# Optimization experiments

Measured on AMD Instinct MI355X. Metric: run time of the kernel, lower is better.

The kernel has to match this reference:

```python
import jax, jax.numpy as jnp
import numpy as np

B, T, N, D = 4, 24, 2048, 128
H = 4
HD = D // H
E = 8
K = 2
INTER = 512            # dim * mlp_ratio
MINTER = INTER // K    # per-expert intermediate (512//2 = 256)
EPS = 1e-6
ALPHA = 0.05           # GCN residual mixing
SCALE = HD ** -0.5


def setup_inputs() -> dict:
    key = jax.random.key(0)
    ks = jax.random.split(key, 32)
    w = lambda i, shape: (jax.random.normal(ks[i], shape, jnp.float32) * 0.02)
    inp = {
        "x": jax.random.normal(ks[0], (B, T, N, D), jnp.float32),
        "k": jax.random.normal(ks[1], (B, T, N, D), jnp.float32),
        "v": jax.random.normal(ks[2], (B, T, N, D), jnp.float32),
        "adj": jax.random.uniform(ks[3], (N, N), jnp.float32),
        # attention qkv projections (torch Linear: y = x @ W.T + b)
        "Wq": w(4, (D, D)), "bq": jnp.zeros((D,), jnp.float32),
        "Wk": w(5, (D, D)), "bk": jnp.zeros((D,), jnp.float32),
        "Wv": w(6, (D, D)), "bv": jnp.zeros((D,), jnp.float32),
        "norm_tatt_w": jnp.ones((D,), jnp.float32),
        # GCN
        "gcn_fc1_w": w(7, (D, D)),
        "gcn_mlp_w": w(8, (D, D)), "gcn_mlp_b": jnp.zeros((D,), jnp.float32),
        # block norms
        "norm1_w": jnp.ones((D,), jnp.float32),
        "norm2_w": jnp.ones((D,), jnp.float32),
        # MoE
        "gate_w": w(9, (E, D)),
        "ew1": w(10, (E, MINTER, D)),
        "ew2": w(11, (E, D, MINTER)),
        "ew3": w(12, (E, MINTER, D)),
        "sw1": w(13, (INTER, D)),
        "sw2": w(14, (D, INTER)),
        "sw3": w(15, (INTER, D)),
        "sgate_w": w(16, (1, D)),
    }
    return inp


def rms_norm(x, w):
    var = jnp.mean(x * x, axis=-1, keepdims=True)
    return w * (x * jax.lax.rsqrt(var + EPS))


def swiglu(x, w1, w2, w3):
    return (jax.nn.silu(x @ w1.T) * (x @ w3.T)) @ w2.T


def reference(x, k, v, adj, Wq, bq, Wk, bk, Wv, bv, norm_tatt_w,
              gcn_fc1_w, gcn_mlp_w, gcn_mlp_b, norm1_w, norm2_w,
              gate_w, ew1, ew2, ew3, sw1, sw2, sw3, sgate_w):
    # ---- pre-norm ----
    x_n = rms_norm(x, norm1_w)
    k_n = rms_norm(k, norm1_w)

    # ---- temporal self-attention (per node, over T) ----
    def heads(y, W, b):  # [B,T,N,D] -> [B,N,H,T,hd]
        y = y @ W.T + b
        return y.transpose(0, 2, 1, 3).reshape(B, N, -1, H, HD).transpose(0, 1, 3, 2, 4)

    q = heads(x_n, Wq, bq)
    kk = heads(k_n, Wk, bk)
    vv = heads(k_n, Wv, bv)  # module passes k for both k and v
    attn = jnp.einsum('bnhqd,bnhkd->bnhqk', q, kk) * SCALE
    attn = jax.nn.softmax(attn, axis=-1)
    t_x = jnp.einsum('bnhqk,bnhkd->bnhqd', attn, vv)
    t_x = t_x.transpose(0, 3, 1, 2, 4).reshape(B, T, N, D)  # [B,T,N,D]
    t_x = rms_norm(t_x, norm_tatt_w)

    # ---- GCN: row-normalized adjacency over node axis ----
    a = adj / jnp.sum(adj, axis=1, keepdims=True)            # a[n,k] = adj[n,k]/d[n]
    mixed = jnp.einsum('nk,btkd->btnd', a, t_x)
    gcn_out = mixed @ gcn_fc1_w.T
    out = ALPHA * t_x + (1.0 - ALPHA) * gcn_out
    ho = out @ gcn_mlp_w.T + gcn_mlp_b

    x = x + ho  # residual (drop_path = identity)

    # ---- MoE sparse experts ----
    x2 = rms_norm(x, norm2_w).reshape(-1, D)                 # [Tok, D]
    router_logits = x2 @ gate_w.T                            # [Tok, E]
    rw = jax.nn.softmax(router_logits.astype(jnp.float32), axis=-1)
    top_w, top_idx = jax.lax.top_k(rw, K)                    # [Tok, K]
    top_w = top_w.astype(x2.dtype)

    final = jnp.zeros_like(x2)
    for e in range(E):  # fixed small expert count
        coef = jnp.sum(jnp.where(top_idx == e, top_w, 0.0), axis=-1)  # [Tok]
        final = final + coef[:, None] * swiglu(x2, ew1[e], ew2[e], ew3[e])

    shared = swiglu(x2, sw1, sw2, sw3)
    shared = jax.nn.sigmoid(x2 @ sgate_w.T) * shared
    final = final + shared

    x = x + final.reshape(B, T, N, D)
    return x, router_logits
```

## Files before the change

### kernel.cpp

```cpp
#include <hip/hip_runtime.h>

#define BB 4
#define TT 24
#define NN 2048
#define DD 128
#define HH 4
#define HD 32
#define TOK 196608
#define EE 8
#define MINTER 256
#define INTER 512

typedef unsigned short u16;
typedef __attribute__((ext_vector_type(8))) short  bf16x8;
typedef __attribute__((ext_vector_type(4))) float  f32x4;
typedef __attribute__((ext_vector_type(4))) unsigned int u32x4;

#define MFMA(a,b,c) __builtin_amdgcn_mfma_f32_16x16x32_bf16((a),(b),(c),0,0,0)
#define AS(n) __attribute__((address_space(n)))

static __device__ __forceinline__ u16 f2b(float f) {
    union { float f; unsigned u; } v; v.f = f;
    unsigned r = v.u + 0x7FFFu + ((v.u >> 16) & 1u);
    return (u16)(r >> 16);
}
static __device__ __forceinline__ u16 f2b_fast(float f) {
    union { float f; unsigned u; } v; v.f = f;
    return (u16)(v.u >> 16);
}
static __device__ __forceinline__ float b2f(u16 b) {
    union { unsigned u; float f; } v; v.u = ((unsigned)b) << 16;
    return v.f;
}
static __device__ __forceinline__ float silu_mul(float u, float v) {
    return u * __builtin_amdgcn_rcpf(1.f + __expf(-u)) * v;
}

template<int C>
static __device__ __forceinline__ bf16x8 frag_ld(const u16* s, int row, int kbyte) {
    constexpr int mask = ((C/8) < 8 ? (C/8) : 8) - 1;
    int byte = row * (C * 2) + (kbyte ^ ((row & mask) << 4));
    return *(const bf16x8*)((const char*)s + byte);
}
template<int C>
static __device__ __forceinline__ u16 lds_us(const u16* s, int r, int c) {
    constexpr int mask = ((C/8) < 8 ? (C/8) : 8) - 1;
    int byte = r * (C * 2) + ((((c >> 3) << 4) ^ ((r & mask) << 4))) + ((c & 7) << 1);
    return *(const u16*)((const char*)s + byte);
}
template<int C>
static __device__ __forceinline__ void lds_store_us(u16* s, int r, int c, u16 v) {
    constexpr int mask = ((C/8) < 8 ? (C/8) : 8) - 1;
    int byte = r * (C * 2) + ((((c >> 3) << 4) ^ ((r & mask) << 4))) + ((c & 7) << 1);
    *(u16*)((char*)s + byte) = v;
}
static __device__ __forceinline__ bf16x8 frag_ld_p80(const u16* s, int row, int kbyte) {
    return *(const bf16x8*)((const char*)s + row * 80 + kbyte);
}
static __device__ __forceinline__ void sh_store_p80(u16* s, int r, int c, u16 v) {
    *(u16*)((char*)s + r * 80 + c * 2) = v;
}
template<int C>
static __device__ __forceinline__ void stage_bf16(u16* s, const u16* g, int gstride,
                                                  int rows, int tid, int nthr) {
    constexpr int cpr = C / 8;
    constexpr int mask = (cpr < 8 ? cpr : 8) - 1;
    for (int i = tid; i < rows * cpr; i += nthr) {
        int r = i / cpr, cc = i - r * cpr;
        u32x4 v = *(const u32x4*)(g + (size_t)r * gstride + cc * 8);
        *(u32x4*)((char*)s + r * (C * 2) + ((cc * 16) ^ ((r & mask) << 4))) = v;
    }
}
static __device__ __forceinline__ void stage_rms(u16* sA, const float* __restrict__ in,
        const float* __restrict__ nw, int tid) {
    int wid = tid >> 6, lane = tid & 63;
    float2 wv = *(const float2*)(nw + lane * 2);
    for (int rr = 0; rr < 32; ++rr) {
        int r = wid * 32 + rr;
        float2 v = *(const float2*)(in + (size_t)r * 128 + lane * 2);
        float ss = v.x * v.x + v.y * v.y;
        #pragma unroll
        for (int o = 32; o > 0; o >>= 1) ss += __shfl_xor(ss, o);
        float sc = rsqrtf(ss * (1.f / 128.f) + 1e-6f);
        unsigned pack = ((unsigned)f2b(v.y * sc * wv.y) << 16) | (unsigned)f2b(v.x * sc * wv.x);
        int byte = r * 256 + (((lane >> 2) * 16) ^ ((r & 7) << 4)) + ((lane & 3) << 2);
        *(unsigned*)((char*)sA + byte) = pack;
    }
}
static __device__ __forceinline__ void stage_async64(u16* s, const u16* g, int wi, int lane) {
    int slot = wi * 64 + lane;
    int r = slot >> 3, c = slot & 7;
    const u16* src = g + r * 2048 + ((c ^ (r & 7)) << 3);
    __builtin_amdgcn_global_load_lds((const AS(1) void*)src,
                                     (AS(3) void*)(s + wi * 512), 16, 0, 0);
}
static __device__ __forceinline__ void stage_img16(u16* buf, const u16* img, int wid, int lane) {
    #pragma unroll
    for (int t = 0; t < 4; ++t) {
        int wi = wid + t * 4;
        __builtin_amdgcn_global_load_lds((const AS(1) void*)(img + wi * 512 + lane * 8),
                                         (AS(3) void*)(buf + wi * 512), 16, 0, 0);
    }
}
static __device__ __forceinline__ void zero_acc(f32x4 acc[4][4]) {
    f32x4 z = {0.f, 0.f, 0.f, 0.f};
    #pragma unroll
    for (int i = 0; i < 4; ++i)
        #pragma unroll
        for (int j = 0; j < 4; ++j) acc[i][j] = z;
}
template<int CA, int CB>
static __device__ __forceinline__ void gemm_step64(const u16* sA, const u16* sB,
        int arow0, int brow0, int kbyte, f32x4 acc[4][4], int ln15) {
    bf16x8 a[4], b[4];
    #pragma unroll
    for (int i = 0; i < 4; ++i) a[i] = frag_ld<CA>(sA, arow0 + i * 16 + ln15, kbyte);
    #pragma unroll
    for (int j = 0; j < 4; ++j) b[j] = frag_ld<CB>(sB, brow0 + j * 16 + ln15, kbyte);
    #pragma unroll
    for (int i = 0; i < 4; ++i)
        #pragma unroll
        for (int j = 0; j < 4; ++j)
            acc[i][j] = MFMA(a[i], b[j], acc[i][j]);
}

static __device__ __forceinline__ void swiglu_chunk(const u16* buf, u16* sH,
        const bf16x8 av[2][4], const bf16x8 w2r[8], f32x4 aout[2][8],
        int wid, int g16, int ln15) {
    const u16* W1c = buf;
    const u16* W3c = buf + 4096;
    f32x4 z = {0.f, 0.f, 0.f, 0.f};
    f32x4 a1[2][2], a3[2][2];
    #pragma unroll
    for (int mf = 0; mf < 2; ++mf)
        #pragma unroll
        for (int nf = 0; nf < 2; ++nf) { a1[mf][nf] = z; a3[mf][nf] = z; }
    __builtin_amdgcn_s_setprio(1);
    #pragma unroll
    for (int ks = 0; ks < 4; ++ks) {
        int kb = ks * 64 + g16 * 16;
        #pragma unroll
        for (int nf = 0; nf < 2; ++nf) {
            bf16x8 b1 = frag_ld<128>(W1c, nf * 16 + ln15, kb);
            bf16x8 b3 = frag_ld<128>(W3c, nf * 16 + ln15, kb);
            a1[0][nf] = MFMA(av[0][ks], b1, a1[0][nf]);
            a1[1][nf] = MFMA(av[1][ks], b1, a1[1][nf]);
            a3[0][nf] = MFMA(av[0][ks], b3, a3[0][nf]);
            a3[1][nf] = MFMA(av[1][ks], b3, a3[1][nf]);
        }
    }
    __builtin_amdgcn_s_setprio(0);
    #pragma unroll
    for (int mf = 0; mf < 2; ++mf)
        #pragma unroll
        for (int nf = 0; nf < 2; ++nf)
            #pragma unroll
            for (int r = 0; r < 4; ++r) {
                int row = wid * 32 + mf * 16 + g16 * 4 + r;
                int col = nf * 16 + ln15;
                sh_store_p80(sH, row, col, f2b_fast(silu_mul(a1[mf][nf][r], a3[mf][nf][r])));
            }
    asm volatile("s_waitcnt lgkmcnt(0)" ::: "memory");
    __builtin_amdgcn_sched_barrier(0);
    {
        int kb = g16 * 16;
        bf16x8 ah0 = frag_ld_p80(sH, wid * 32 + ln15, kb);
        bf16x8 ah1 = frag_ld_p80(sH, wid * 32 + 16 + ln15, kb);
        __builtin_amdgcn_s_setprio(1);
        #pragma unroll
        for (int nf = 0; nf < 8; ++nf) {
            aout[0][nf] = MFMA(ah0, w2r[nf], aout[0][nf]);
            aout[1][nf] = MFMA(ah1, w2r[nf], aout[1][nf]);
        }
        __builtin_amdgcn_s_setprio(0);
    }
}

__global__ __launch_bounds__(256) void preconvert(
        const float* __restrict__ Wq, const float* __restrict__ Wk,
        const float* __restrict__ Wv, const float* __restrict__ g1,
        const float* __restrict__ g2,
        const float* __restrict__ e1, const float* __restrict__ e2,
        const float* __restrict__ e3,
        const float* __restrict__ s1, const float* __restrict__ s2,
        const float* __restrict__ s3,
        u16* __restrict__ arena, int* __restrict__ cnts) {
    int idx = blockIdx.x * 256 + threadIdx.x;
    if (blockIdx.x == 0 && threadIdx.x < 8) cnts[threadIdx.x] = 0;
    if (idx < 20480) {
        int s = idx >> 12, rel = idx & 4095;
        const float* src = (s == 0) ? Wq : (s == 1) ? Wk : (s == 2) ? Wv : (s == 3) ? g1 : g2;
        const float4 v = *(const float4*)(src + (size_t)rel * 4);
        union { unsigned long long q; u16 us[4]; } o;
        o.us[0] = f2b(v.x); o.us[1] = f2b(v.y); o.us[2] = f2b(v.z); o.us[3] = f2b(v.w);
        *(unsigned long long*)(arena + (size_t)idx * 4) = o.q;
        return;
    }
    int p = idx - 20480;
    if (p >= 122880) return;
    int imgIdx = p / 1536;
    int ppos = p - imgIdx * 1536;
    const float *w1s, *w3s, *w2s_; int w2stride, ic;
    u16* img;
    if (imgIdx < 64) {
        int e = imgIdx >> 3; ic = imgIdx & 7;
        w1s = e1 + (size_t)e * 32768;
        w3s = e3 + (size_t)e * 32768;
        w2s_ = e2 + (size_t)e * 32768;
        w2stride = 256;
        img = arena + 81920 + (size_t)imgIdx * 12288;
    } else {
        ic = imgIdx - 64;
        w1s = s1; w3s = s3; w2s_ = s2; w2stride = 512;
        img = arena + 868352 + (size_t)ic * 12288;
    }
    const float* src;
    if (ppos < 1024) {
        const float* wsrc = (ppos < 512) ? w1s : w3s;
        int pp = ppos & 511;
        int r = pp >> 4, chq = pp & 15;
        int cc = chq ^ (r & 7);
        src = wsrc + (size_t)(ic * 32 + r) * 128 + cc * 8;
    } else {
        int q = ppos - 1024;
        int nf = q >> 6, ln = q & 63;
        int l15 = ln & 15, g = ln >> 4;
        src = w2s_ + (size_t)(nf * 16 + l15) * w2stride + ic * 32 + g * 8;
    }
    union { u32x4 v; u16 us[8]; } o;
    #pragma unroll
    for (int j = 0; j < 8; ++j) o.us[j] = f2b(src[j]);
    *(u32x4*)(img + (size_t)ppos * 8) = o.v;
}

__global__ __launch_bounds__(256) void proj_rms(
        const float* __restrict__ xin, const u16* __restrict__ W,
        const float* __restrict__ bias, const float* __restrict__ nw,
        u16* __restrict__ out) {
    int tok0 = blockIdx.x * 128;
    __shared__ u16 sA[128 * 128];
    __shared__ u16 sW[128 * 128];
    int tid = threadIdx.x, lane = tid & 63, ln15 = lane & 15, g16 = lane >> 4, wid = tid >> 6;
    int wm = (wid >> 1) * 64, wn = (wid & 1) * 64;
    stage_rms(sA, xin + (size_t)tok0 * 128, nw, tid);
    stage_bf16<128>(sW, W, 128, 128, tid, 256);
    __syncthreads();
    f32x4 acc[4][4];
    zero_acc(acc);
    #pragma unroll
    for (int ks = 0; ks < 4; ++ks)
        gemm_step64<128, 128>(sA, sW, wm, wn, ks * 64 + g16 * 16, acc, ln15);
    #pragma unroll
    for (int j = 0; j < 4; ++j) {
        int col = wn + j * 16 + ln15;
        float bv = bias[col];
        #pragma unroll
        for (int i = 0; i < 4; ++i)
            #pragma unroll
            for (int r = 0; r < 4; ++r) {
                int row = wm + i * 16 + g16 * 4 + r;
                out[(size_t)(tok0 + row) * 128 + col] = f2b(acc[i][j][r] + bv);
            }
    }
}

__global__ __launch_bounds__(256) void projkv_rms(
        const float* __restrict__ kin, const u16* __restrict__ Wk,
        const float* __restrict__ bk, const u16* __restrict__ Wv,
        const float* __restrict__ bv, const float* __restrict__ nw,
        u16* __restrict__ kout, u16* __restrict__ vout) {
    int tok0 = blockIdx.x * 128;
    __shared__ u16 sA[128 * 128];
    __shared__ u16 sW[128 * 128];
    int tid = threadIdx.x, lane = tid & 63, ln15 = lane & 15, g16 = lane >> 4, wid = tid >> 6;
    int wm = (wid >> 1) * 64, wn = (wid & 1) * 64;
    stage_rms(sA, kin + (size_t)tok0 * 128, nw, tid);
    stage_bf16<128>(sW, Wk, 128, 128, tid, 256);
    __syncthreads();
    f32x4 acc[4][4];
    zero_acc(acc);
    #pragma unroll
    for (int ks = 0; ks < 4; ++ks)
        gemm_step64<128, 128>(sA, sW, wm, wn, ks * 64 + g16 * 16, acc, ln15);
    #pragma unroll
    for (int j = 0; j < 4; ++j) {
        int col = wn + j * 16 + ln15;
        float bvv = bk[col];
        #pragma unroll
        for (int i = 0; i < 4; ++i)
            #pragma unroll
            for (int r = 0; r < 4; ++r) {
                int row = wm + i * 16 + g16 * 4 + r;
                kout[(size_t)(tok0 + row) * 128 + col] = f2b(acc[i][j][r] + bvv);
            }
    }
    __syncthreads();
    stage_bf16<128>(sW, Wv, 128, 128, tid, 256);
    __syncthreads();
    zero_acc(acc);
    #pragma unroll
    for (int ks = 0; ks < 4; ++ks)
        gemm_step64<128, 128>(sA, sW, wm, wn, ks * 64 + g16 * 16, acc, ln15);
    #pragma unroll
    for (int j = 0; j < 4; ++j) {
        int col = wn + j * 16 + ln15;
        float bvv = bv[col];
        #pragma unroll
        for (int i = 0; i < 4; ++i)
            #pragma unroll
            for (int r = 0; r < 4; ++r) {
                int row = wm + i * 16 + g16 * 4 + r;
                vout[(size_t)(tok0 + row) * 128 + col] = f2b(acc[i][j][r] + bvv);
            }
    }
}

__global__ __launch_bounds__(256) void attn_kernel(
        const u16* __restrict__ q, const u16* __restrict__ kk, const u16* __restrict__ vv,
        const float* __restrict__ ntw, u16* __restrict__ txn) {
    int bid = blockIdx.x;
    int b = bid >> 11;
    int n = bid & 2047;
    __shared__ u16 sQ[4][24][32];
    __shared__ u16 sK[4][24][32];
    __shared__ u16 sV[4][24][32];
    __shared__ float sS[4][24][24];
    __shared__ float sO[24][128];
    int tid = threadIdx.x, lane = tid & 63, wid = tid >> 6;
    for (int idx = tid; idx < 3072; idx += 256) {
        int h = idx / 768;
        int rem = idx - h * 768;
        int t = rem >> 5;
        int d = rem & 31;
        size_t off = ((size_t)((b * 24 + t) * 2048 + n)) * 128 + h * 32 + d;
        sQ[h][t][d] = q[off];
        sK[h][t][d] = kk[off];
        sV[h][t][d] = vv[off];
    }
    __syncthreads();
    int h = wid;
    for (int i = lane; i < 576; i += 64) {
        int qi = i / 24, ki = i - qi * 24;
        float s = 0.f;
        #pragma unroll
        for (int c = 0; c < 32; ++c) s += b2f(sQ[h][qi][c]) * b2f(sK[h][ki][c]);
        sS[h][qi][ki] = s * 0.17677669529663687f;
    }
    __syncthreads();
    if (lane < 24) {
        float m = -1e30f;
        #pragma unroll
        for (int c = 0; c < 24; ++c) m = fmaxf(m, sS[h][lane][c]);
        float e[24]; float sum = 0.f;
        #pragma unroll
        for (int c = 0; c < 24; ++c) { e[c] = __expf(sS[h][lane][c] - m); sum += e[c]; }
        float inv = 1.f / sum;
        #pragma unroll
        for (int c = 0; c < 24; ++c) sS[h][lane][c] = e[c] * inv;
    }
    __syncthreads();
    for (int i = lane; i < 768; i += 64) {
        int qi = i >> 5, d = i & 31;
        float acc = 0.f;
        #pragma unroll
        for (int c = 0; c < 24; ++c) acc += sS[h][qi][c] * b2f(sV[h][c][d]);
        sO[qi][h * 32 + d] = acc;
    }
    __syncthreads();
    for (int j = 0; j < 6; ++j) {
        int t = wid * 6 + j;
        float v0 = sO[t][lane], v1 = sO[t][lane + 64];
        float ss = v0 * v0 + v1 * v1;
        #pragma unroll
        for (int o = 32; o > 0; o >>= 1) ss += __shfl_xor(ss, o);
        float sc = rsqrtf(ss * (1.f / 128.f) + 1e-6f);
        size_t off = ((size_t)((b * 24 + t) * 2048 + n)) * 128;
        txn[off + lane]      = f2b(v0 * sc * ntw[lane]);
        txn[off + lane + 64] = f2b(v1 * sc * ntw[lane + 64]);
    }
}

__global__ __launch_bounds__(256) void adj_norm(const float* __restrict__ adj, u16* __restrict__ abf) {
    int nrow = blockIdx.x;
    const float* r = adj + (size_t)nrow * 2048;
    int tid = threadIdx.x;
    float s = 0.f;
    for (int c = tid; c < 2048; c += 256) s += r[c];
    __shared__ float red[4];
    #pragma unroll
    for (int o = 32; o > 0; o >>= 1) s += __shfl_xor(s, o);
    if ((tid & 63) == 0) red[tid >> 6] = s;
    __syncthreads();
    float inv = 1.f / (red[0] + red[1] + red[2] + red[3]);
    u16* o = abf + (size_t)nrow * 2048;
    for (int c = tid; c < 2048; c += 256) o[c] = f2b(r[c] * inv);
}

__global__ __launch_bounds__(256) void transpose_k(const u16* __restrict__ txn, u16* __restrict__ txT) {
    int bt = blockIdx.x >> 5;
    int n0 = (blockIdx.x & 31) * 64;
    int tid = threadIdx.x;
    int nn = tid & 63, dg = tid >> 6;
    for (int rep = 0; rep < 4; ++rep) {
        int d0 = rep * 32 + dg * 8;
        union { u32x4 v; u16 us[8]; } u;
        u.v = *(const u32x4*)(txn + ((size_t)(bt * 2048 + n0 + nn)) * 128 + d0);
        #pragma unroll
        for (int j = 0; j < 8; ++j)
            txT[((size_t)(bt * 128 + d0 + j)) * 2048 + n0 + nn] = u.us[j];
    }
}

__global__ __launch_bounds__(256) void gcn_gemm(
        const u16* __restrict__ abf, const u16* __restrict__ txT, u16* __restrict__ mixed) {
    int bt = blockIdx.x >> 4;
    int n0 = (blockIdx.x & 15) * 128;
    __shared__ u16 sA[128 * 64];
    __shared__ u16 sB[128 * 64];
    int tid = threadIdx.x, lane = tid & 63, ln15 = lane & 15, g16 = lane >> 4, wid = tid >> 6;
    int wm = (wid >> 1) * 64, wn = (wid & 1) * 64;
    f32x4 acc[4][4];
    zero_acc(acc);
    const u16* aRow = abf + (size_t)n0 * 2048;
    const u16* bRow = txT + (size_t)bt * 128 * 2048;
    for (int k0 = 0; k0 < 2048; k0 += 64) {
        __syncthreads();
        #pragma unroll
        for (int i = 0; i < 4; ++i) stage_async64(sA, aRow + k0, wid * 4 + i, lane);
        #pragma unroll
        for (int i = 0; i < 4; ++i) stage_async64(sB, bRow + k0, wid * 4 + i, lane);
        __syncthreads();
        #pragma unroll
        for (int ks = 0; ks < 2; ++ks)
            gemm_step64<64, 64>(sA, sB, wm, wn, ks * 64 + g16 * 16, acc, ln15);
    }
    u16* out = mixed + ((size_t)(bt * 2048 + n0)) * 128;
    #pragma unroll
    for (int i = 0; i < 4; ++i)
        #pragma unroll
        for (int j = 0; j < 4; ++j)
            #pragma unroll
            for (int r = 0; r < 4; ++r) {
                int row = wm + i * 16 + g16 * 4 + r;
                int col = wn + j * 16 + ln15;
                out[(size_t)row * 128 + col] = f2b(acc[i][j][r]);
            }
}

__global__ __launch_bounds__(256) void fused_gcn_router(
        const u16* __restrict__ mixed, const u16* __restrict__ txn,
        const float* __restrict__ x,
        const u16* __restrict__ W1, const u16* __restrict__ W2,
        const float* __restrict__ bias2, const float* __restrict__ n2w,
        const float* __restrict__ gatew,
        float* __restrict__ outx, float* __restrict__ outlog,
        u16* __restrict__ x2n,
        int* __restrict__ lists, float* __restrict__ listw, int* __restrict__ cnts) {
    int tok0 = blockIdx.x * 128;
    __shared__ char LB[65536];
    __shared__ float sGate[1024];
    __shared__ float sN2[128];
    __shared__ float sBias[128];
    __shared__ float sLog[1024];
    __shared__ float sPart[256];
    __shared__ float sScale[128];
    __shared__ int sBCnt[8];
    __shared__ int sGBase[8];
    u16* sM = (u16*)LB;
    u16* sW = (u16*)(LB + 32768);
    float* sXn = (float*)LB;
    int tid = threadIdx.x, lane = tid & 63, ln15 = lane & 15, g16 = lane >> 4, wid = tid >> 6;
    int wm = (wid >> 1) * 64, wn = (wid & 1) * 64;
    stage_bf16<128>(sM, mixed + (size_t)tok0 * 128, 128, 128, tid, 256);
    stage_bf16<128>(sW, W1, 128, 128, tid, 256);
    for (int i = tid; i < 1024; i += 256) sGate[i] = gatew[i];
    if (tid < 128) { sN2[tid] = n2w[tid]; sBias[tid] = bias2[tid]; }
    if (tid < 8) sBCnt[tid] = 0;
    __syncthreads();
    f32x4 acc[4][4];
    zero_acc(acc);
    #pragma unroll
    for (int ks = 0; ks < 4; ++ks)
        gemm_step64<128, 128>(sM, sW, wm, wn, ks * 64 + g16 * 16, acc, ln15);
    __syncthreads();
    stage_bf16<128>(sM, txn + (size_t)tok0 * 128, 128, 128, tid, 256);
    stage_bf16<128>(sW, W2, 128, 128, tid, 256);
    __syncthreads();
    #pragma unroll
    for (int i = 0; i < 4; ++i)
        #pragma unroll
        for (int j = 0; j < 4; ++j)
            #pragma unroll
            for (int r = 0; r < 4; ++r) {
                int row = wm + i * 16 + g16 * 4 + r;
                int col = wn + j * 16 + ln15;
                float tv = b2f(lds_us<128>(sM, row, col));
                lds_store_us<128>(sM, row, col, f2b(0.05f * tv + 0.95f * acc[i][j][r]));
            }
    __syncthreads();
    zero_acc(acc);
    #pragma unroll
    for (int ks = 0; ks < 4; ++ks)
        gemm_step64<128, 128>(sM, sW, wm, wn, ks * 64 + g16 * 16, acc, ln15);
    #pragma unroll
    for (int i = 0; i < 4; ++i)
        #pragma unroll
        for (int j = 0; j < 4; ++j)
            #pragma unroll
            for (int r = 0; r < 4; ++r) {
                int row = wm + i * 16 + g16 * 4 + r;
                int col = wn + j * 16 + ln15;
                float xv = x[(size_t)(tok0 + row) * 128 + col] + acc[i][j][r] + sBias[col];
                outx[(size_t)(tok0 + row) * 128 + col] = xv;
                acc[i][j][r] = xv;
            }
    #pragma unroll
    for (int i = 0; i < 4; ++i)
        #pragma unroll
        for (int r = 0; r < 4; ++r) {
            float s = 0.f;
            #pragma unroll
            for (int j = 0; j < 4; ++j) s += acc[i][j][r] * acc[i][j][r];
            s += __shfl_xor(s, 1); s += __shfl_xor(s, 2);
            s += __shfl_xor(s, 4); s += __shfl_xor(s, 8);
            if (ln15 == 0) sPart[(wm + i * 16 + g16 * 4 + r) * 2 + (wid & 1)] = s;
        }
    __syncthreads();
    if (tid < 128)
        sScale[tid] = rsqrtf((sPart[tid * 2] + sPart[tid * 2 + 1]) * (1.f / 128.f) + 1e-6f);
    __syncthreads();
    #pragma unroll
    for (int i = 0; i < 4; ++i)
        #pragma unroll
        for (int j = 0; j < 4; ++j)
            #pragma unroll
            for (int r = 0; r < 4; ++r) {
                int row = wm + i * 16 + g16 * 4 + r;
                int col = wn + j * 16 + ln15;
                sXn[row * 128 + col] = acc[i][j][r] * sScale[row] * sN2[col];
            }
    __syncthreads();
    {
        int r = tid >> 1, e0 = (tid & 1) * 4;
        float a0 = 0, a1 = 0, a2 = 0, a3 = 0;
        for (int cc = 0; cc < 128; ++cc) {
            int c = (cc + r) & 127;
            float v = sXn[r * 128 + c];
            a0 += v * sGate[(e0 + 0) * 128 + c];
            a1 += v * sGate[(e0 + 1) * 128 + c];
            a2 += v * sGate[(e0 + 2) * 128 + c];
            a3 += v * sGate[(e0 + 3) * 128 + c];
        }
        int rb = r * 8 + e0;
        sLog[rb + 0] = a0; sLog[rb + 1] = a1; sLog[rb + 2] = a2; sLog[rb + 3] = a3;
        size_t ob = (size_t)(tok0 + r) * 8 + e0;
        outlog[ob + 0] = a0; outlog[ob + 1] = a1; outlog[ob + 2] = a2; outlog[ob + 3] = a3;
    }
    for (int cc = tid; cc < 2048; cc += 256) {
        int r = cc >> 4, c0 = (cc & 15) * 8;
        union { u32x4 v; u16 us[8]; } u;
        #pragma unroll
        for (int jj = 0; jj < 8; ++jj) u.us[jj] = f2b(sXn[r * 128 + c0 + jj]);
        *(u32x4*)(x2n + (size_t)(tok0 + r) * 128 + c0) = u.v;
    }
    __syncthreads();
    int e1 = 0, e2 = 0, le1 = 0, le2 = 0;
    float w1v = 0.f, w2v = 0.f;
    if (tid < 128) {
        int r = tid;
        float l[8];
        #pragma unroll
        for (int e = 0; e < 8; ++e) l[e] = sLog[r * 8 + e];
        float m = l[0];
        #pragma unroll
        for (int e = 1; e < 8; ++e) m = fmaxf(m, l[e]);
        float ex[8]; float s = 0.f;
        #pragma unroll
        for (int e = 0; e < 8; ++e) { ex[e] = __expf(l[e] - m); s += ex[e]; }
        float inv = 1.f / s;
        float b1v = ex[0]; e1 = 0;
        #pragma unroll
        for (int e = 1; e < 8; ++e) if (ex[e] > b1v) { b1v = ex[e]; e1 = e; }
        e2 = (e1 == 0) ? 1 : 0; float b2v = ex[e2];
        #pragma unroll
        for (int e = 0; e < 8; ++e) if (e != e1 && ex[e] > b2v) { b2v = ex[e]; e2 = e; }
        w1v = b1v * inv; w2v = b2v * inv;
        le1 = atomicAdd(&sBCnt[e1], 1);
        le2 = atomicAdd(&sBCnt[e2], 1);
    }
    __syncthreads();
    if (tid < 8) sGBase[tid] = atomicAdd(&cnts[tid], sBCnt[tid]);
    __syncthreads();
    if (tid < 128) {
        int tok = tok0 + tid;
        int p1 = sGBase[e1] + le1;
        lists[(size_t)e1 * TOK + p1] = tok * 2 + 0; listw[(size_t)e1 * TOK + p1] = w1v;
        int p2 = sGBase[e2] + le2;
        lists[(size_t)e2 * TOK + p2] = tok * 2 + 1; listw[(size_t)e2 * TOK + p2] = w2v;
    }
}

__global__ __launch_bounds__(256, 2) void moe_expert(
        const u16* __restrict__ x2n, const int* __restrict__ lists,
        const float* __restrict__ listw, const int* __restrict__ cnts,
        const u16* __restrict__ eimg, u16* __restrict__ slotOut) {
    int e = blockIdx.y;
    int base = blockIdx.x * 128;
    int cnt = cnts[e];
    if (base >= cnt) return;
    int valid = min(128, cnt - base);
    const int* lst = lists + (size_t)e * TOK + base;
    const float* lw = listw + (size_t)e * TOK + base;
    __shared__ u16 sBufA[8192];
    __shared__ u16 sBufB[8192];
    __shared__ u16 sH[5120];
    __shared__ float sCoef[128];
    __shared__ int sTok[128];
    int tid = threadIdx.x, lane = tid & 63, ln15 = lane & 15, g16 = lane >> 4, wid = tid >> 6;
    const u16* imgbase = eimg + (size_t)(e * 8) * 12288;
    stage_img16(sBufA, imgbase, wid, lane);
    if (tid < 128) {
        int t = (tid < valid) ? lst[tid] : -1;
        sTok[tid] = t;
        sCoef[tid] = (tid < valid) ? lw[tid] : 0.f;
    }
    __syncthreads();
    bf16x8 av[2][4];
    {
        bf16x8 zz = {0, 0, 0, 0, 0, 0, 0, 0};
        int t0 = sTok[wid * 32 + ln15];
        int t1 = sTok[wid * 32 + 16 + ln15];
        const u16* r0 = x2n + (size_t)(t0 >> 1) * 128;
        const u16* r1 = x2n + (size_t)(t1 >> 1) * 128;
        #pragma unroll
        for (int ks = 0; ks < 4; ++ks) {
            av[0][ks] = (t0 >= 0) ? *(const bf16x8*)(r0 + ks * 32 + g16 * 8) : zz;
            av[1][ks] = (t1 >= 0) ? *(const bf16x8*)(r1 + ks * 32 + g16 * 8) : zz;
        }
    }
    f32x4 aout[2][8];
    f32x4 z = {0.f, 0.f, 0.f, 0.f};
    #pragma unroll
    for (int mf = 0; mf < 2; ++mf)
        #pragma unroll
        for (int nf = 0; nf < 8; ++nf) aout[mf][nf] = z;
    for (int ic = 0; ic < 8; ++ic) {
        u16* cur = (ic & 1) ? sBufB : sBufA;
        u16* alt = (ic & 1) ? sBufA : sBufB;
        bf16x8 w2r[8];
        const u16* w2img = imgbase + (size_t)ic * 12288 + 8192;
        #pragma unroll
        for (int nf = 0; nf < 8; ++nf)
            w2r[nf] = *(const bf16x8*)(w2img + nf * 512 + lane * 8);
        if (ic + 1 < 8)
            stage_img16(alt, imgbase + (size_t)(ic + 1) * 12288, wid, lane);
        swiglu_chunk(cur, sH, av, w2r, aout, wid, g16, ln15);
        __syncthreads();
    }
    #pragma unroll
    for (int mf = 0; mf < 2; ++mf)
        #pragma unroll
        for (int nf = 0; nf < 8; ++nf)
            #pragma unroll
            for (int r = 0; r < 4; ++r) {
                int row = wid * 32 + mf * 16 + g16 * 4 + r;
                if (row < valid) {
                    int col = nf * 16 + ln15;
                    slotOut[(size_t)sTok[row] * 128 + col] = f2b_fast(sCoef[row] * aout[mf][nf][r]);
                }
            }
}

__global__ __launch_bounds__(256, 2) void moe_shared(
        const u16* __restrict__ x2n, const u16* __restrict__ simg,
        const float* __restrict__ sgw, const u16* __restrict__ slotOut,
        float* __restrict__ outx) {
    int tok0 = blockIdx.x * 128;
    __shared__ u16 sBufA[8192];
    __shared__ u16 sBufB[8192];
    __shared__ u16 sH[5120];
    __shared__ float sGv[128];
    int tid = threadIdx.x, lane = tid & 63, ln15 = lane & 15, g16 = lane >> 4, wid = tid >> 6;
    stage_img16(sBufA, simg, wid, lane);
    bf16x8 av[2][4];
    {
        const u16* r0 = x2n + (size_t)(tok0 + wid * 32 + ln15) * 128;
        const u16* r1 = x2n + (size_t)(tok0 + wid * 32 + 16 + ln15) * 128;
        #pragma unroll
        for (int ks = 0; ks < 4; ++ks) {
            av[0][ks] = *(const bf16x8*)(r0 + ks * 32 + g16 * 8);
            av[1][ks] = *(const bf16x8*)(r1 + ks * 32 + g16 * 8);
        }
    }
    if (tid < 128) {
        const u16* xr = x2n + (size_t)(tok0 + tid) * 128;
        float d = 0.f;
        #pragma unroll
        for (int c8 = 0; c8 < 16; ++c8) {
            bf16x8 v = *(const bf16x8*)(xr + c8 * 8);
            #pragma unroll
            for (int j = 0; j < 8; ++j) d += b2f((u16)v[j]) * sgw[c8 * 8 + j];
        }
        sGv[tid] = 1.f / (1.f + __expf(-d));
    }
    f32x4 aout[2][8];
    f32x4 z = {0.f, 0.f, 0.f, 0.f};
    #pragma unroll
    for (int mf = 0; mf < 2; ++mf)
        #pragma unroll
        for (int nf = 0; nf < 8; ++nf) aout[mf][nf] = z;
    __syncthreads();
    for (int ic = 0; ic < 16; ++ic) {
        u16* cur = (ic & 1) ? sBufB : sBufA;
        u16* alt = (ic & 1) ? sBufA : sBufB;
        bf16x8 w2r[8];
        const u16* w2img = simg + (size_t)ic * 12288 + 8192;
        #pragma unroll
        for (int nf = 0; nf < 8; ++nf)
            w2r[nf] = *(const bf16x8*)(w2img + nf * 512 + lane * 8);
        if (ic + 1 < 16)
            stage_img16(alt, simg + (size_t)(ic + 1) * 12288, wid, lane);
        swiglu_chunk(cur, sH, av, w2r, aout, wid, g16, ln15);
        __syncthreads();
    }
    #pragma unroll
    for (int mf = 0; mf < 2; ++mf)
        #pragma unroll
        for (int nf = 0; nf < 8; ++nf)
            #pragma unroll
            for (int r = 0; r < 4; ++r) {
                int row = wid * 32 + mf * 16 + g16 * 4 + r;
                int col = nf * 16 + ln15;
                size_t t = (size_t)(tok0 + row);
                float fc = b2f(slotOut[(t * 2 + 0) * 128 + col])
                         + b2f(slotOut[(t * 2 + 1) * 128 + col]);
                size_t idx = t * 128 + col;
                outx[idx] = outx[idx] + fc + sGv[row] * aout[mf][nf][r];
            }
}

#define SZTD  ((size_t)TOK * 128 * 2)
#define OFF_XN   ((size_t)0)
#define OFF_KN   (SZTD)
#define OFF_Q    (SZTD * 2)
#define OFF_KP   (SZTD * 3)
#define OFF_VP   (SZTD * 4)
#define OFF_ABF  (SZTD * 5)
#define OFF_LW   (OFF_ABF + 8388608)
#define OFF_LIST (OFF_LW + (size_t)8 * TOK * 4)
#define OFF_CNT  (OFF_LIST + (size_t)8 * TOK * 4)
#define OFF_ARENA (OFF_CNT + 128)

extern "C" void kernel_launch(void* const* d_in, const int* in_sizes, int n_in,
                              void* d_out, int out_size, void* d_ws, size_t ws_size,
                              hipStream_t stream) {
    (void)in_sizes; (void)n_in; (void)out_size; (void)ws_size;
    const float* x    = (const float*)d_in[0];
    const float* k    = (const float*)d_in[1];
    const float* adj  = (const float*)d_in[3];
    const float* Wq   = (const float*)d_in[4];
    const float* bq   = (const float*)d_in[5];
    const float* Wk   = (const float*)d_in[6];
    const float* bk   = (const float*)d_in[7];
    const float* Wv   = (const float*)d_in[8];
    const float* bv   = (const float*)d_in[9];
    const float* ntw  = (const float*)d_in[10];
    const float* gfc1 = (const float*)d_in[11];
    const float* gmlp = (const float*)d_in[12];
    const float* gmlpb= (const float*)d_in[13];
    const float* n1w  = (const float*)d_in[14];
    const float* n2w  = (const float*)d_in[15];
    const float* gatew= (const float*)d_in[16];
    const float* ew1  = (const float*)d_in[17];
    const float* ew2  = (const float*)d_in[18];
    const float* ew3  = (const float*)d_in[19];
    const float* sw1  = (const float*)d_in[20];
    const float* sw2  = (const float*)d_in[21];
    const float* sw3  = (const float*)d_in[22];
    const float* sgw  = (const float*)d_in[23];

    char* ws = (char*)d_ws;
    u16*  xn   = (u16*)(ws + OFF_XN);
    u16*  kn   = (u16*)(ws + OFF_KN);
    u16*  qb   = (u16*)(ws + OFF_Q);
    u16*  kpb  = (u16*)(ws + OFF_KP);
    u16*  vpb  = (u16*)(ws + OFF_VP);
    u16*  slotOut = (u16*)(ws + OFF_KP);
    u16*  abf  = (u16*)(ws + OFF_ABF);
    float* lw  = (float*)(ws + OFF_LW);
    int*  lst  = (int*)(ws + OFF_LIST);
    int*  cnts = (int*)(ws + OFF_CNT);
    u16*  arena = (u16*)(ws + OFF_ARENA);
    u16*  bWq = arena;
    u16*  bWk = arena + 16384;
    u16*  bWv = arena + 32768;
    u16*  bG1 = arena + 49152;
    u16*  bG2 = arena + 65536;
    u16*  eimg = arena + 81920;
    u16*  simg = arena + 868352;
    float* outx   = (float*)d_out;
    float* outlog = outx + (size_t)TOK * 128;

    preconvert<<<560, 256, 0, stream>>>(Wq, Wk, Wv, gfc1, gmlp, ew1, ew2, ew3,
                                        sw1, sw2, sw3, arena, cnts);
    proj_rms<<<1536, 256, 0, stream>>>(x, bWq, bq, n1w, qb);
    projkv_rms<<<1536, 256, 0, stream>>>(k, bWk, bk, bWv, bv, n1w, kpb, vpb);
    attn_kernel<<<8192, 256, 0, stream>>>(qb, kpb, vpb, ntw, xn );
    adj_norm<<<2048, 256, 0, stream>>>(adj, abf);
    transpose_k<<<3072, 256, 0, stream>>>(xn, qb );
    gcn_gemm<<<1536, 256, 0, stream>>>(abf, qb, kn );
    fused_gcn_router<<<1536, 256, 0, stream>>>(kn, xn, x, bG1, bG2, gmlpb, n2w, gatew,
                                               outx, outlog, qb , lst, lw, cnts);
    moe_expert<<<dim3(1536, 8), 256, 0, stream>>>(qb, lst, lw, cnts, eimg, slotOut);
    moe_shared<<<1536, 256, 0, stream>>>(qb, simg, sgw, slotOut, outx);
}
```

Baseline: 738.9 us.

## Software-pipeline SwiGLU chunks so W1/W3 MFMA overlaps previous chunk's activation and W2

The per-chunk SwiGLU is split into a first phase (W1/W3 MFMAs into registers) and a finish phase (silu-mul, write to shared H, W2 MFMA). Both MoE kernels now run a skewed pipeline: the first phase of chunk i+1 is issued before the finish phase of chunk i, using two register accumulator sets. The goal is to hide the latency of the shared-memory round trip and the W2 global loads behind independent MFMA work. In exchange it doubles the live accumulator registers, which may raise register pressure under launch_bounds(256,2), and the prologue and epilogue are unrolled by hand.

```diff
diff --git a/kernel.cpp b/kernel.cpp
--- a/kernel.cpp
+++ b/kernel.cpp
@@ -124,13 +124,11 @@
             acc[i][j] = MFMA(a[i], b[j], acc[i][j]);
 }
 
-static __device__ __forceinline__ void swiglu_chunk(const u16* buf, u16* sH,
-        const bf16x8 av[2][4], const bf16x8 w2r[8], f32x4 aout[2][8],
-        int wid, int g16, int ln15) {
+static __device__ __forceinline__ void p1_phase(const u16* buf, const bf16x8 av[2][4],
+        f32x4 a1[2][2], f32x4 a3[2][2], int g16, int ln15) {
     const u16* W1c = buf;
     const u16* W3c = buf + 4096;
     f32x4 z = {0.f, 0.f, 0.f, 0.f};
-    f32x4 a1[2][2], a3[2][2];
     #pragma unroll
     for (int mf = 0; mf < 2; ++mf)
         #pragma unroll
@@ -150,6 +148,14 @@
         }
     }
     __builtin_amdgcn_s_setprio(0);
+}
+static __device__ __forceinline__ void finish_phase(const f32x4 a1[2][2], const f32x4 a3[2][2],
+        const u16* w2img, u16* sH, f32x4 aout[2][8],
+        int wid, int g16, int ln15, int lane) {
+    bf16x8 w2r[8];
+    #pragma unroll
+    for (int nf = 0; nf < 8; ++nf)
+        w2r[nf] = *(const bf16x8*)(w2img + nf * 512 + lane * 8);
     #pragma unroll
     for (int mf = 0; mf < 2; ++mf)
         #pragma unroll
@@ -644,19 +650,29 @@
     for (int mf = 0; mf < 2; ++mf)
         #pragma unroll
         for (int nf = 0; nf < 8; ++nf) aout[mf][nf] = z;
-    for (int ic = 0; ic < 8; ++ic) {
-        u16* cur = (ic & 1) ? sBufB : sBufA;
-        u16* alt = (ic & 1) ? sBufA : sBufB;
-        bf16x8 w2r[8];
-        const u16* w2img = imgbase + (size_t)ic * 12288 + 8192;
-        #pragma unroll
-        for (int nf = 0; nf < 8; ++nf)
-            w2r[nf] = *(const bf16x8*)(w2img + nf * 512 + lane * 8);
-        if (ic + 1 < 8)
-            stage_img16(alt, imgbase + (size_t)(ic + 1) * 12288, wid, lane);
-        swiglu_chunk(cur, sH, av, w2r, aout, wid, g16, ln15);
+    f32x4 a1A[2][2], a3A[2][2], a1B[2][2], a3B[2][2];
+    stage_img16(sBufB, imgbase + 12288, wid, lane);
+    p1_phase(sBufA, av, a1A, a3A, g16, ln15);
+    __syncthreads();
+    #pragma unroll 1
+    for (int icp = 0; icp < 3; ++icp) {
+        int ic1 = 2 * icp + 1;
+        stage_img16(sBufA, imgbase + (size_t)(ic1 + 1) * 12288, wid, lane);
+        p1_phase(sBufB, av, a1B, a3B, g16, ln15);
+        finish_phase(a1A, a3A, imgbase + (size_t)(ic1 - 1) * 12288 + 8192,
+                     sH, aout, wid, g16, ln15, lane);
         __syncthreads();
-    }
+        int ic2 = 2 * icp + 2;
+        stage_img16(sBufB, imgbase + (size_t)(ic2 + 1) * 12288, wid, lane);
+        p1_phase(sBufA, av, a1A, a3A, g16, ln15);
+        finish_phase(a1B, a3B, imgbase + (size_t)(ic2 - 1) * 12288 + 8192,
+                     sH, aout, wid, g16, ln15, lane);
+        __syncthreads();
+    }
+    p1_phase(sBufB, av, a1B, a3B, g16, ln15);
+    finish_phase(a1A, a3A, imgbase + (size_t)6 * 12288 + 8192, sH, aout, wid, g16, ln15, lane);
+    __syncthreads();
+    finish_phase(a1B, a3B, imgbase + (size_t)7 * 12288 + 8192, sH, aout, wid, g16, ln15, lane);
     #pragma unroll
     for (int mf = 0; mf < 2; ++mf)
         #pragma unroll
@@ -710,19 +726,29 @@
         #pragma unroll
         for (int nf = 0; nf < 8; ++nf) aout[mf][nf] = z;
     __syncthreads();
-    for (int ic = 0; ic < 16; ++ic) {
-        u16* cur = (ic & 1) ? sBufB : sBufA;
-        u16* alt = (ic & 1) ? sBufA : sBufB;
-        bf16x8 w2r[8];
-        const u16* w2img = simg + (size_t)ic * 12288 + 8192;
-        #pragma unroll
-        for (int nf = 0; nf < 8; ++nf)
-            w2r[nf] = *(const bf16x8*)(w2img + nf * 512 + lane * 8);
-        if (ic + 1 < 16)
-            stage_img16(alt, simg + (size_t)(ic + 1) * 12288, wid, lane);
-        swiglu_chunk(cur, sH, av, w2r, aout, wid, g16, ln15);
+    f32x4 a1A[2][2], a3A[2][2], a1B[2][2], a3B[2][2];
+    stage_img16(sBufB, simg + 12288, wid, lane);
+    p1_phase(sBufA, av, a1A, a3A, g16, ln15);
+    __syncthreads();
+    #pragma unroll 1
+    for (int icp = 0; icp < 7; ++icp) {
+        int ic1 = 2 * icp + 1;
+        stage_img16(sBufA, simg + (size_t)(ic1 + 1) * 12288, wid, lane);
+        p1_phase(sBufB, av, a1B, a3B, g16, ln15);
+        finish_phase(a1A, a3A, simg + (size_t)(ic1 - 1) * 12288 + 8192,
+                     sH, aout, wid, g16, ln15, lane);
         __syncthreads();
-    }
+        int ic2 = 2 * icp + 2;
+        stage_img16(sBufB, simg + (size_t)(ic2 + 1) * 12288, wid, lane);
+        p1_phase(sBufA, av, a1A, a3A, g16, ln15);
+        finish_phase(a1B, a3B, simg + (size_t)(ic2 - 1) * 12288 + 8192,
+                     sH, aout, wid, g16, ln15, lane);
+        __syncthreads();
+    }
+    p1_phase(sBufB, av, a1B, a3B, g16, ln15);
+    finish_phase(a1A, a3A, simg + (size_t)14 * 12288 + 8192, sH, aout, wid, g16, ln15, lane);
+    __syncthreads();
+    finish_phase(a1B, a3B, simg + (size_t)15 * 12288 + 8192, sH, aout, wid, g16, ln15, lane);
     #pragma unroll
     for (int mf = 0; mf < 2; ++mf)
         #pragma unroll
```

After: 742.2 us. Within noise of the previous version (+0.5%).

## Double-buffer GCN GEMM tiles and split MoE blocks into 8 waves

Applied to the files above, without the earlier changes.

The GCN GEMM now ping-pongs between two shared-memory tile buffers, so async loads of the next K-slab overlap the MFMAs on the current one and there is one barrier per slab instead of two. The MoE expert and shared kernels move from 256 to 512 threads per block, with each wave handling 16 token rows instead of 32. This halves per-wave register fragments (av, aout) and spreads weight staging over 8 waves. The cost is less reuse of each weight fragment per wave, more waves contending for LDS reads of weight chunks, and double the shared memory in the GCN kernel, which may reduce its occupancy.

```diff
diff --git a/kernel.cpp b/kernel.cpp
--- a/kernel.cpp
+++ b/kernel.cpp
@@ -94,10 +94,10 @@
     __builtin_amdgcn_global_load_lds((const AS(1) void*)src,
                                      (AS(3) void*)(s + wi * 512), 16, 0, 0);
 }
-static __device__ __forceinline__ void stage_img16(u16* buf, const u16* img, int wid, int lane) {
-    #pragma unroll
-    for (int t = 0; t < 4; ++t) {
-        int wi = wid + t * 4;
+static __device__ __forceinline__ void stage_img8(u16* buf, const u16* img, int wid, int lane) {
+    #pragma unroll
+    for (int t = 0; t < 2; ++t) {
+        int wi = wid + t * 8;
         __builtin_amdgcn_global_load_lds((const AS(1) void*)(img + wi * 512 + lane * 8),
                                          (AS(3) void*)(buf + wi * 512), 16, 0, 0);
     }
@@ -124,17 +124,15 @@
             acc[i][j] = MFMA(a[i], b[j], acc[i][j]);
 }
 
-static __device__ __forceinline__ void swiglu_chunk(const u16* buf, u16* sH,
-        const bf16x8 av[2][4], const bf16x8 w2r[8], f32x4 aout[2][8],
+static __device__ __forceinline__ void swiglu_chunk8(const u16* buf, u16* sH,
+        const bf16x8 av[4], const bf16x8 w2r[8], f32x4 aout[8],
         int wid, int g16, int ln15) {
     const u16* W1c = buf;
     const u16* W3c = buf + 4096;
     f32x4 z = {0.f, 0.f, 0.f, 0.f};
-    f32x4 a1[2][2], a3[2][2];
-    #pragma unroll
-    for (int mf = 0; mf < 2; ++mf)
-        #pragma unroll
-        for (int nf = 0; nf < 2; ++nf) { a1[mf][nf] = z; a3[mf][nf] = z; }
+    f32x4 a1[2], a3[2];
+    #pragma unroll
+    for (int nf = 0; nf < 2; ++nf) { a1[nf] = z; a3[nf] = z; }
     __builtin_amdgcn_s_setprio(1);
     #pragma unroll
     for (int ks = 0; ks < 4; ++ks) {
@@ -143,35 +141,28 @@
         for (int nf = 0; nf < 2; ++nf) {
             bf16x8 b1 = frag_ld<128>(W1c, nf * 16 + ln15, kb);
             bf16x8 b3 = frag_ld<128>(W3c, nf * 16 + ln15, kb);
-            a1[0][nf] = MFMA(av[0][ks], b1, a1[0][nf]);
-            a1[1][nf] = MFMA(av[1][ks], b1, a1[1][nf]);
-            a3[0][nf] = MFMA(av[0][ks], b3, a3[0][nf]);
-            a3[1][nf] = MFMA(av[1][ks], b3, a3[1][nf]);
+            a1[nf] = MFMA(av[ks], b1, a1[nf]);
+            a3[nf] = MFMA(av[ks], b3, a3[nf]);
         }
     }
     __builtin_amdgcn_s_setprio(0);
     #pragma unroll
-    for (int mf = 0; mf < 2; ++mf)
-        #pragma unroll
-        for (int nf = 0; nf < 2; ++nf)
-            #pragma unroll
-            for (int r = 0; r < 4; ++r) {
-                int row = wid * 32 + mf * 16 + g16 * 4 + r;
-                int col = nf * 16 + ln15;
-                sh_store_p80(sH, row, col, f2b_fast(silu_mul(a1[mf][nf][r], a3[mf][nf][r])));
-            }
+    for (int nf = 0; nf < 2; ++nf)
+        #pragma unroll
+        for (int r = 0; r < 4; ++r) {
+            int row = wid * 16 + g16 * 4 + r;
+            int col = nf * 16 + ln15;
+            sh_store_p80(sH, row, col, f2b_fast(silu_mul(a1[nf][r], a3[nf][r])));
+        }
     asm volatile("s_waitcnt lgkmcnt(0)" ::: "memory");
     __builtin_amdgcn_sched_barrier(0);
     {
         int kb = g16 * 16;
-        bf16x8 ah0 = frag_ld_p80(sH, wid * 32 + ln15, kb);
-        bf16x8 ah1 = frag_ld_p80(sH, wid * 32 + 16 + ln15, kb);
+        bf16x8 ah = frag_ld_p80(sH, wid * 16 + ln15, kb);
         __builtin_amdgcn_s_setprio(1);
         #pragma unroll
-        for (int nf = 0; nf < 8; ++nf) {
-            aout[0][nf] = MFMA(ah0, w2r[nf], aout[0][nf]);
-            aout[1][nf] = MFMA(ah1, w2r[nf], aout[1][nf]);
-        }
+        for (int nf = 0; nf < 8; ++nf)
+            aout[nf] = MFMA(ah, w2r[nf], aout[nf]);
         __builtin_amdgcn_s_setprio(0);
     }
 }
@@ -415,24 +406,40 @@
         const u16* __restrict__ abf, const u16* __restrict__ txT, u16* __restrict__ mixed) {
     int bt = blockIdx.x >> 4;
     int n0 = (blockIdx.x & 15) * 128;
-    __shared__ u16 sA[128 * 64];
-    __shared__ u16 sB[128 * 64];
+    __shared__ u16 sA0[8192];
+    __shared__ u16 sB0[8192];
+    __shared__ u16 sA1[8192];
+    __shared__ u16 sB1[8192];
     int tid = threadIdx.x, lane = tid & 63, ln15 = lane & 15, g16 = lane >> 4, wid = tid >> 6;
     int wm = (wid >> 1) * 64, wn = (wid & 1) * 64;
     f32x4 acc[4][4];
     zero_acc(acc);
     const u16* aRow = abf + (size_t)n0 * 2048;
     const u16* bRow = txT + (size_t)bt * 128 * 2048;
-    for (int k0 = 0; k0 < 2048; k0 += 64) {
+    #pragma unroll
+    for (int i = 0; i < 4; ++i) stage_async64(sA0, aRow, wid * 4 + i, lane);
+    #pragma unroll
+    for (int i = 0; i < 4; ++i) stage_async64(sB0, bRow, wid * 4 + i, lane);
+    __syncthreads();
+    for (int kk = 0; kk < 2048; kk += 128) {
+        #pragma unroll
+        for (int i = 0; i < 4; ++i) stage_async64(sA1, aRow + kk + 64, wid * 4 + i, lane);
+        #pragma unroll
+        for (int i = 0; i < 4; ++i) stage_async64(sB1, bRow + kk + 64, wid * 4 + i, lane);
+        #pragma unroll
+        for (int ks = 0; ks < 2; ++ks)
+            gemm_step64<64, 64>(sA0, sB0, wm, wn, ks * 64 + g16 * 16, acc, ln15);
         __syncthreads();
-        #pragma unroll
-        for (int i = 0; i < 4; ++i) stage_async64(sA, aRow + k0, wid * 4 + i, lane);
-        #pragma unroll
-        for (int i = 0; i < 4; ++i) stage_async64(sB, bRow + k0, wid * 4 + i, lane);
+        if (kk + 128 < 2048) {
+            #pragma unroll
+            for (int i = 0; i < 4; ++i) stage_async64(sA0, aRow + kk + 128, wid * 4 + i, lane);
+            #pragma unroll
+            for (int i = 0; i < 4; ++i) stage_async64(sB0, bRow + kk + 128, wid * 4 + i, lane);
+        }
+        #pragma unroll
+        for (int ks = 0; ks < 2; ++ks)
+            gemm_step64<64, 64>(sA1, sB1, wm, wn, ks * 64 + g16 * 16, acc, ln15);
         __syncthreads();
-        #pragma unroll
-        for (int ks = 0; ks < 2; ++ks)
-            gemm_step64<64, 64>(sA, sB, wm, wn, ks * 64 + g16 * 16, acc, ln15);
     }
     u16* out = mixed + ((size_t)(bt * 2048 + n0)) * 128;
     #pragma unroll
@@ -600,7 +607,7 @@
     }
 }
 
-__global__ __launch_bounds__(256, 2) void moe_expert(
+__global__ __launch_bounds__(512, 2) void moe_expert(
         const u16* __restrict__ x2n, const int* __restrict__ lists,
         const float* __restrict__ listw, const int* __restrict__ cnts,
         const u16* __restrict__ eimg, u16* __restrict__ slotOut) {
@@ -618,32 +625,26 @@
     __shared__ int sTok[128];
     int tid = threadIdx.x, lane = tid & 63, ln15 = lane & 15, g16 = lane >> 4, wid = tid >> 6;
     const u16* imgbase = eimg + (size_t)(e * 8) * 12288;
-    stage_img16(sBufA, imgbase, wid, lane);
+    stage_img8(sBufA, imgbase, wid, lane);
     if (tid < 128) {
         int t = (tid < valid) ? lst[tid] : -1;
         sTok[tid] = t;
         sCoef[tid] = (tid < valid) ? lw[tid] : 0.f;
     }
     __syncthreads();
-    bf16x8 av[2][4];
+    bf16x8 av[4];
     {
         bf16x8 zz = {0, 0, 0, 0, 0, 0, 0, 0};
-        int t0 = sTok[wid * 32 + ln15];
-        int t1 = sTok[wid * 32 + 16 + ln15];
+        int t0 = sTok[wid * 16 + ln15];
         const u16* r0 = x2n + (size_t)(t0 >> 1) * 128;
-        const u16* r1 = x2n + (size_t)(t1 >> 1) * 128;
-        #pragma unroll
-        for (int ks = 0; ks < 4; ++ks) {
-            av[0][ks] = (t0 >= 0) ? *(const bf16x8*)(r0 + ks * 32 + g16 * 8) : zz;
-            av[1][ks] = (t1 >= 0) ? *(const bf16x8*)(r1 + ks * 32 + g16 * 8) : zz;
-        }
-    }
-    f32x4 aout[2][8];
+        #pragma unroll
+        for (int ks = 0; ks < 4; ++ks)
+            av[ks] = (t0 >= 0) ? *(const bf16x8*)(r0 + ks * 32 + g16 * 8) : zz;
+    }
+    f32x4 aout[8];
     f32x4 z = {0.f, 0.f, 0.f, 0.f};
     #pragma unroll
-    for (int mf = 0; mf < 2; ++mf)
-        #pragma unroll
-        for (int nf = 0; nf < 8; ++nf) aout[mf][nf] = z;
+    for (int nf = 0; nf < 8; ++nf) aout[nf] = z;
     for (int ic = 0; ic < 8; ++ic) {
         u16* cur = (ic & 1) ? sBufB : sBufA;
         u16* alt = (ic & 1) ? sBufA : sBufB;
@@ -653,25 +654,23 @@
         for (int nf = 0; nf < 8; ++nf)
             w2r[nf] = *(const bf16x8*)(w2img + nf * 512 + lane * 8);
         if (ic + 1 < 8)
-            stage_img16(alt, imgbase + (size_t)(ic + 1) * 12288, wid, lane);
-        swiglu_chunk(cur, sH, av, w2r, aout, wid, g16, ln15);
+            stage_img8(alt, imgbase + (size_t)(ic + 1) * 12288, wid, lane);
+        swiglu_chunk8(cur, sH, av, w2r, aout, wid, g16, ln15);
         __syncthreads();
     }
     #pragma unroll
-    for (int mf = 0; mf < 2; ++mf)
-        #pragma unroll
-        for (int nf = 0; nf < 8; ++nf)
-            #pragma unroll
-            for (int r = 0; r < 4; ++r) {
-                int row = wid * 32 + mf * 16 + g16 * 4 + r;
-                if (row < valid) {
-                    int col = nf * 16 + ln15;
-                    slotOut[(size_t)sTok[row] * 128 + col] = f2b_fast(sCoef[row] * aout[mf][nf][r]);
-                }
+    for (int nf = 0; nf < 8; ++nf)
+        #pragma unroll
+        for (int r = 0; r < 4; ++r) {
+            int row = wid * 16 + g16 * 4 + r;
+            if (row < valid) {
+                int col = nf * 16 + ln15;
+                slotOut[(size_t)sTok[row] * 128 + col] = f2b_fast(sCoef[row] * aout[nf][r]);
             }
-}
-
-__global__ __launch_bounds__(256, 2) void moe_shared(
+        }
+}
+
+__global__ __launch_bounds__(512, 2) void moe_shared(
         const u16* __restrict__ x2n, const u16* __restrict__ simg,
         const float* __restrict__ sgw, const u16* __restrict__ slotOut,
         float* __restrict__ outx) {
@@ -681,16 +680,13 @@
     __shared__ u16 sH[5120];
     __shared__ float sGv[128];
     int tid = threadIdx.x, lane = tid & 63, ln15 = lane & 15, g16 = lane >> 4, wid = tid >> 6;
-    stage_img16(sBufA, simg, wid, lane);
-    bf16x8 av[2][4];
+    stage_img8(sBufA, simg, wid, lane);
+    bf16x8 av[4];
     {
-        const u16* r0 = x2n + (size_t)(tok0 + wid * 32 + ln15) * 128;
-        const u16* r1 = x2n + (size_t)(tok0 + wid * 32 + 16 + ln15) * 128;
-        #pragma unroll
-        for (int ks = 0; ks < 4; ++ks) {
-            av[0][ks] = *(const bf16x8*)(r0 + ks * 32 + g16 * 8);
-            av[1][ks] = *(const bf16x8*)(r1 + ks * 32 + g16 * 8);
-        }
+        const u16* r0 = x2n + (size_t)(tok0 + wid * 16 + ln15) * 128;
+        #pragma unroll
+        for (int ks = 0; ks < 4; ++ks)
+            av[ks] = *(const bf16x8*)(r0 + ks * 32 + g16 * 8);
     }
     if (tid < 128) {
         const u16* xr = x2n + (size_t)(tok0 + tid) * 128;
@@ -703,12 +699,10 @@
         }
         sGv[tid] = 1.f / (1.f + __expf(-d));
     }
-    f32x4 aout[2][8];
+    f32x4 aout[8];
     f32x4 z = {0.f, 0.f, 0.f, 0.f};
     #pragma unroll
-    for (int mf = 0; mf < 2; ++mf)
-        #pragma unroll
-        for (int nf = 0; nf < 8; ++nf) aout[mf][nf] = z;
+    for (int nf = 0; nf < 8; ++nf) aout[nf] = z;
     __syncthreads();
     for (int ic = 0; ic < 16; ++ic) {
         u16* cur = (ic & 1) ? sBufB : sBufA;
@@ -719,24 +713,22 @@
         for (int nf = 0; nf < 8; ++nf)
             w2r[nf] = *(const bf16x8*)(w2img + nf * 512 + lane * 8);
         if (ic + 1 < 16)
-            stage_img16(alt, simg + (size_t)(ic + 1) * 12288, wid, lane);
-        swiglu_chunk(cur, sH, av, w2r, aout, wid, g16, ln15);
+            stage_img8(alt, simg + (size_t)(ic + 1) * 12288, wid, lane);
+        swiglu_chunk8(cur, sH, av, w2r, aout, wid, g16, ln15);
         __syncthreads();
     }
     #pragma unroll
-    for (int mf = 0; mf < 2; ++mf)
-        #pragma unroll
-        for (int nf = 0; nf < 8; ++nf)
-            #pragma unroll
-            for (int r = 0; r < 4; ++r) {
-                int row = wid * 32 + mf * 16 + g16 * 4 + r;
-                int col = nf * 16 + ln15;
-                size_t t = (size_t)(tok0 + row);
-                float fc = b2f(slotOut[(t * 2 + 0) * 128 + col])
-                         + b2f(slotOut[(t * 2 + 1) * 128 + col]);
-                size_t idx = t * 128 + col;
-                outx[idx] = outx[idx] + fc + sGv[row] * aout[mf][nf][r];
-            }
+    for (int nf = 0; nf < 8; ++nf)
+        #pragma unroll
+        for (int r = 0; r < 4; ++r) {
+            int row = wid * 16 + g16 * 4 + r;
+            int col = nf * 16 + ln15;
+            size_t t = (size_t)(tok0 + row);
+            float fc = b2f(slotOut[(t * 2 + 0) * 128 + col])
+                     + b2f(slotOut[(t * 2 + 1) * 128 + col]);
+            size_t idx = t * 128 + col;
+            outx[idx] = outx[idx] + fc + sGv[row] * aout[nf][r];
+        }
 }
 
 #define SZTD  ((size_t)TOK * 128 * 2)
@@ -811,6 +803,6 @@
     gcn_gemm<<<1536, 256, 0, stream>>>(abf, qb, kn );
     fused_gcn_router<<<1536, 256, 0, stream>>>(kn, xn, x, bG1, bG2, gmlpb, n2w, gatew,
                                                outx, outlog, qb , lst, lw, cnts);
-    moe_expert<<<dim3(1536, 8), 256, 0, stream>>>(qb, lst, lw, cnts, eimg, slotOut);
-    moe_shared<<<1536, 256, 0, stream>>>(qb, simg, sgw, slotOut, outx);
-}
+    moe_expert<<<dim3(1536, 8), 512, 0, stream>>>(qb, lst, lw, cnts, eimg, slotOut);
+    moe_shared<<<1536, 512, 0, stream>>>(qb, simg, sgw, slotOut, outx);
+}
```

Result: slower. 788.5 us (+6.7%).
